# Optimization experiments

Hardware: AMD Instinct MI355X
Metric: run time of the kernel (lower is better)

## Reference

```python
import jax, jax.numpy as jnp
import numpy as np
from jax import lax

B, ENC, H, E, V = 16, 64, 96, 128, 32000

def _same_pad(k):
    # PyTorch padding='same' (stride=1): low = (k-1)//2, high = (k-1) - low
    t = k - 1
    return (t // 2, t - t // 2)

def _conv(x, w, pad):
    return lax.conv_general_dilated(x, w, (1, 1), pad,
                                    dimension_numbers=('NCHW', 'OIHW', 'NCHW'))

def setup_inputs() -> dict:
    key = jax.random.key(0)
    ks = jax.random.split(key, 16)
    s = 0.05
    return {
        'encoder_outputs': jax.random.normal(ks[0], (B, ENC, H), jnp.float32),
        'input_ids': jax.random.randint(ks[1], (B,), 0, V),
        'hidden': jax.random.normal(ks[2], (1, B, H), jnp.float32),
        'coverage': jnp.zeros((B, ENC), jnp.float32),
        'emb': jax.random.normal(ks[3], (V, E), jnp.float32) * s,
        'W_dec': jax.random.normal(ks[4], (H, H), jnp.float32) * s,
        'b_dec': jnp.zeros((H,), jnp.float32),
        'attn_w': jax.random.normal(ks[5], (ENC, ENC, H, H), jnp.float32) * 0.003,
        'attn_b': jnp.zeros((ENC,), jnp.float32),
        'cvg_w': jax.random.normal(ks[6], (ENC, ENC, 1, H), jnp.float32) * s,
        'cvg_b': jnp.zeros((ENC,), jnp.float32),
        'v': jax.random.normal(ks[7], (B, H), jnp.float32) * s,
        'W_new': jax.random.normal(ks[8], (H, H + E), jnp.float32) * s,
        'b_new': jnp.zeros((H,), jnp.float32),
        'w_ih': jax.random.normal(ks[9], (3 * H, H), jnp.float32) * s,
        'w_hh': jax.random.normal(ks[10], (3 * H, H), jnp.float32) * s,
        'b_ih': jnp.zeros((3 * H,), jnp.float32),
        'b_hh': jnp.zeros((3 * H,), jnp.float32),
        'W_pre': jax.random.normal(ks[11], (H, 2 * H), jnp.float32) * s,
        'b_pre': jnp.zeros((H,), jnp.float32),
        'W_out': jax.random.normal(ks[12], (V, H), jnp.float32) * s,
        'b_out': jnp.zeros((V,), jnp.float32),
    }

def _attn(hidden, enc_out, coverage, W_dec, b_dec, attn_w, attn_b, cvg_w, cvg_b, v):
    # AttnCalc.forward
    ph, pw = _same_pad(H), _same_pad(H)
    enc_feat = _conv(enc_out.reshape(B, ENC, 1, H), attn_w, (ph, pw))
    enc_feat = enc_feat + attn_b[None, :, None, None]          # (B,ENC,1,H)
    dec_feat = (hidden[0] @ W_dec.T + b_dec).reshape(B, 1, 1, H)
    cvg_feat = _conv(coverage.reshape(B, ENC, 1, 1), cvg_w, ((0, 0), _same_pad(H)))
    cvg_feat = cvg_feat + cvg_b[None, :, None, None]           # (B,ENC,1,1)
    feats = jnp.tanh((enc_feat + dec_feat + cvg_feat).reshape(B, ENC, H))
    attn_weights = jax.nn.softmax(jnp.einsum('beh,bh->be', feats, v), axis=1)
    new_cov = coverage + attn_weights                          # in-place += in torch
    ctx = jnp.einsum('be,beh->bh', attn_weights, enc_out)      # (B,H)
    return ctx, attn_weights, new_cov

def reference(encoder_outputs, input_ids, hidden, coverage, emb, W_dec, b_dec,
              attn_w, attn_b, cvg_w, cvg_b, v, W_new, b_new,
              w_ih, w_hh, b_ih, b_hh, W_pre, b_pre, W_out, b_out):
    embedded = emb[input_ids]                                  # (B,E); dropout = identity (eval)
    ctx1, _, cov1 = _attn(hidden, encoder_outputs, coverage,
                          W_dec, b_dec, attn_w, attn_b, cvg_w, cvg_b, v)
    x = jnp.concatenate([embedded, ctx1], axis=1) @ W_new.T + b_new   # (B,H)
    # single GRU step (PyTorch gate order: r, z, n)
    h = hidden[0]
    gi = x @ w_ih.T + b_ih
    gh = h @ w_hh.T + b_hh
    r = jax.nn.sigmoid(gi[:, :H] + gh[:, :H])
    z = jax.nn.sigmoid(gi[:, H:2 * H] + gh[:, H:2 * H])
    n = jnp.tanh(gi[:, 2 * H:] + r * gh[:, 2 * H:])
    h_new = (1.0 - z) * n + z * h                              # (B,H)
    hidden_new = h_new[None]                                   # (1,B,H)
    ctx2, aw2, cov2 = _attn(hidden_new, encoder_outputs, cov1,
                            W_dec, b_dec, attn_w, attn_b, cvg_w, cvg_b, v)
    o = jnp.tanh(jnp.concatenate([h_new, ctx2], axis=1) @ W_pre.T + b_pre)
    logp = jax.nn.log_softmax(o @ W_out.T + b_out, axis=1)     # (B,V)
    return (logp, hidden_new, ctx2, aw2, cov2)
```

## Files before the change

kernel.cpp:

```cpp
#include <hip/hip_runtime.h>

#define BB 16
#define ENC 64
#define HH 96
#define EE 128
#define VV 32000

__device__ __forceinline__ float tanh_fast(float x) {
    float e = __expf(2.f * x);
    return 1.f - 2.f / (e + 1.f);
}
__device__ __forceinline__ float sigmoid_fast(float x) {
    return 1.f / (1.f + __expf(-x));
}

__global__ __launch_bounds__(128) void k_encfeat(
    const float* __restrict__ enc,
    const float* __restrict__ attn_w,
    const float* __restrict__ cvg_w,
    float* __restrict__ part,
    float* __restrict__ cvgw47)
{
    int blk = blockIdx.x;
    int b   = blk >> 6;
    int ot  = (blk >> 3) & 7;
    int ic  = blk & 7;
    int o0  = ot * 8;
    int i0  = ic * 8;
    int t   = threadIdx.x;

    __shared__ __align__(16) float encS[8 * 192];
    __shared__ __align__(16) float Wb[8 * 8 * 100];

    for (int f = t; f < 8 * 192; f += 128) encS[f] = 0.f;
    __syncthreads();
    for (int f = t; f < 8 * 96; f += 128) {
        int i = f / 96, j = f - i * 96;
        encS[i * 192 + 47 + j] = enc[(size_t)((b * ENC + i0 + i) * 96) + j];
    }
    for (int f4 = t; f4 < 1536; f4 += 128) {
        int o = f4 / 192;
        int r = f4 - o * 192;
        int i = r / 24, kq = r - i * 24;
        float4 q = *(const float4*)(attn_w +
            (size_t)((o0 + o) * ENC + (i0 + i)) * (96 * 96) + 47 * 96 + 4 * kq);
        *(float4*)&Wb[(i * 8 + o) * 100 + 4 * kq] = q;
    }
    if (b == 0 && ot == 0) {
        #pragma unroll
        for (int j = 0; j < 4; ++j) {
            int e = ic * 512 + j * 128 + t;
            cvgw47[e] = cvg_w[(size_t)e * 96 + 47];
        }
    }
    __syncthreads();

    if (t < 96) {
        int og = t & 7;
        int x0 = (t >> 3) * 8;
        float4 a0 = make_float4(0.f, 0.f, 0.f, 0.f);
        float4 a1 = make_float4(0.f, 0.f, 0.f, 0.f);
        for (int i = 0; i < 8; ++i) {
            const float* er = &encS[i * 192 + x0];
            const float* wr = &Wb[(i * 8 + og) * 100];
            float4 eA = *(const float4*)(er);
            float4 eB = *(const float4*)(er + 4);
            #pragma unroll 4
            for (int c = 0; c < 24; ++c) {
                float4 eC = *(const float4*)(er + 4 * c + 8);
                float4 q  = *(const float4*)(wr + 4 * c);
                a0.x += q.x * eA.x + q.y * eA.y + q.z * eA.z + q.w * eA.w;
                a0.y += q.x * eA.y + q.y * eA.z + q.z * eA.w + q.w * eB.x;
                a0.z += q.x * eA.z + q.y * eA.w + q.z * eB.x + q.w * eB.y;
                a0.w += q.x * eA.w + q.y * eB.x + q.z * eB.y + q.w * eB.z;
                a1.x += q.x * eB.x + q.y * eB.y + q.z * eB.z + q.w * eB.w;
                a1.y += q.x * eB.y + q.y * eB.z + q.z * eB.w + q.w * eC.x;
                a1.z += q.x * eB.z + q.y * eB.w + q.z * eC.x + q.w * eC.y;
                a1.w += q.x * eB.w + q.y * eC.x + q.z * eC.y + q.w * eC.z;
                eA = eB; eB = eC;
            }
        }
        float* outr = part + ((size_t)(ic * 16 + b) * 64 + o0 + og) * 96 + x0;
        *(float4*)(outr)     = a0;
        *(float4*)(outr + 4) = a1;
    }
}

__device__ __forceinline__ void matvec4(int g, int q, int nout, int nk,
    const float* __restrict__ W, int ldw, const float* __restrict__ bias,
    const float* __restrict__ xv, float* __restrict__ y)
{
    for (int j = g; j < nout; j += 64) {
        const float* wr = W + (size_t)j * ldw;
        float s = 0.f;
        for (int m = q; m < nk / 4; m += 4) {
            float4 wq = *(const float4*)(wr + 4 * m);
            s += wq.x * xv[4 * m] + wq.y * xv[4 * m + 1]
               + wq.z * xv[4 * m + 2] + wq.w * xv[4 * m + 3];
        }
        s += __shfl_xor(s, 1);
        s += __shfl_xor(s, 2);
        if (q == 0) y[j] = s + bias[j];
    }
}

__global__ __launch_bounds__(256) void k_fused(
    const float* __restrict__ enc, const int* __restrict__ ids,
    const float* __restrict__ hidden, const float* __restrict__ coverage,
    const float* __restrict__ emb,
    const float* __restrict__ W_dec, const float* __restrict__ b_dec,
    const float* __restrict__ attn_b,
    const float* __restrict__ cvgw47, const float* __restrict__ cvg_b,
    const float* __restrict__ vvec,
    const float* __restrict__ W_new, const float* __restrict__ b_new,
    const float* __restrict__ w_ih, const float* __restrict__ w_hh,
    const float* __restrict__ b_ih, const float* __restrict__ b_hh,
    const float* __restrict__ W_pre, const float* __restrict__ b_pre,
    const float* __restrict__ part, float* __restrict__ oG,
    float* __restrict__ out_hidden, float* __restrict__ out_ctx2,
    float* __restrict__ out_aw2, float* __restrict__ out_cov2)
{
    int b = blockIdx.x, t = threadIdx.x;
    int g = t >> 2, q = t & 3;

    __shared__ __align__(16) float efS[ENC * HH];
    __shared__ __align__(16) float encS[ENC * HH];
    __shared__ float hS[HH], vS[HH], decS[HH], ctxS[HH], xS[HH], h2S[HH], ctx2S[HH];
    __shared__ float covS[ENC], cvgS[ENC], sS[ENC], awS[ENC];
    __shared__ float embS[EE];
    __shared__ __align__(16) float xcatS[EE + HH];
    __shared__ float giS[3 * HH], ghS[3 * HH];

    {
        const float4* enc4 = (const float4*)(enc + (size_t)b * ENC * HH);
        float4* efS4  = (float4*)efS;
        float4* encS4 = (float4*)encS;
        for (int f = t; f < (ENC * HH) / 4; f += 256) {
            float4 s = make_float4(0.f, 0.f, 0.f, 0.f);
            #pragma unroll
            for (int ic = 0; ic < 8; ++ic) {
                const float4 p = *(const float4*)(part +
                    (size_t)(ic * 16 + b) * (ENC * HH) + 4 * f);
                s.x += p.x; s.y += p.y; s.z += p.z; s.w += p.w;
            }
            efS4[f]  = s;
            encS4[f] = enc4[f];
        }
    }
    if (t < HH) { hS[t] = hidden[b * HH + t]; vS[t] = vvec[b * HH + t]; }
    if (t >= 96 && t < 160) covS[t - 96] = coverage[b * ENC + (t - 96)];
    if (t >= 128 && t < 256) embS[t - 128] = emb[(size_t)ids[b] * EE + (t - 128)];
    __syncthreads();

    matvec4(g, q, HH, HH, W_dec, HH, b_dec, hS, decS);
    matvec4(g, q, ENC, ENC, cvgw47, ENC, cvg_b, covS, cvgS);
    __syncthreads();
    {
        int e = g;
        float base = attn_b[e] + cvgS[e];
        const float* efr = &efS[e * HH];
        float s = 0.f;
        for (int m = q; m < 24; m += 4) {
            #pragma unroll
            for (int u = 0; u < 4; ++u) {
                int xx = 4 * m + u;
                s += tanh_fast(efr[xx] + decS[xx] + base) * vS[xx];
            }
        }
        s += __shfl_xor(s, 1); s += __shfl_xor(s, 2);
        if (q == 0) sS[e] = s;
    }
    __syncthreads();
    if (t < ENC) {
        float m = -1e30f;
        for (int j = 0; j < ENC; ++j) m = fmaxf(m, sS[j]);
        float sum = 0.f;
        for (int j = 0; j < ENC; ++j) sum += __expf(sS[j] - m);
        float aw = __expf(sS[t] - m) / sum;
        awS[t] = aw;
        covS[t] += aw;
    }
    __syncthreads();
    if (t < HH) {
        float c = 0.f;
        for (int o = 0; o < ENC; ++o) c += awS[o] * encS[o * HH + t];
        ctxS[t] = c;
        xcatS[EE + t] = c;
    }
    if (t >= 128 && t < 256) xcatS[t - 128] = embS[t - 128];
    __syncthreads();

    matvec4(g, q, HH, EE + HH, W_new, EE + HH, b_new, xcatS, xS);
    __syncthreads();

    matvec4(g, q, 3 * HH, HH, w_ih, HH, b_ih, xS, giS);
    matvec4(g, q, 3 * HH, HH, w_hh, HH, b_hh, hS, ghS);
    __syncthreads();
    if (t < HH) {
        float r = sigmoid_fast(giS[t] + ghS[t]);
        float z = sigmoid_fast(giS[HH + t] + ghS[HH + t]);
        float n = tanh_fast(giS[2 * HH + t] + r * ghS[2 * HH + t]);
        float hn = (1.f - z) * n + z * hS[t];
        h2S[t] = hn;
        out_hidden[b * HH + t] = hn;
    }
    __syncthreads();

    matvec4(g, q, HH, HH, W_dec, HH, b_dec, h2S, decS);
    matvec4(g, q, ENC, ENC, cvgw47, ENC, cvg_b, covS, cvgS);
    __syncthreads();
    {
        int e = g;
        float base = attn_b[e] + cvgS[e];
        const float* efr = &efS[e * HH];
        float s = 0.f;
        for (int m = q; m < 24; m += 4) {
            #pragma unroll
            for (int u = 0; u < 4; ++u) {
                int xx = 4 * m + u;
                s += tanh_fast(efr[xx] + decS[xx] + base) * vS[xx];
            }
        }
        s += __shfl_xor(s, 1); s += __shfl_xor(s, 2);
        if (q == 0) sS[e] = s;
    }
    __syncthreads();
    if (t < ENC) {
        float m = -1e30f;
        for (int j = 0; j < ENC; ++j) m = fmaxf(m, sS[j]);
        float sum = 0.f;
        for (int j = 0; j < ENC; ++j) sum += __expf(sS[j] - m);
        float aw = __expf(sS[t] - m) / sum;
        awS[t] = aw;
        covS[t] += aw;
        out_aw2[b * ENC + t]  = aw;
        out_cov2[b * ENC + t] = covS[t];
    }
    __syncthreads();
    if (t < HH) {
        float c = 0.f;
        for (int o = 0; o < ENC; ++o) c += awS[o] * encS[o * HH + t];
        ctx2S[t] = c;
        out_ctx2[b * HH + t] = c;
        xcatS[t] = h2S[t];
        xcatS[HH + t] = c;
    }
    __syncthreads();

    for (int j = g; j < HH; j += 64) {
        const float* wr = W_pre + (size_t)j * (2 * HH);
        float s = 0.f;
        for (int m = q; m < (2 * HH) / 4; m += 4) {
            float4 wq = *(const float4*)(wr + 4 * m);
            s += wq.x * xcatS[4 * m] + wq.y * xcatS[4 * m + 1]
               + wq.z * xcatS[4 * m + 2] + wq.w * xcatS[4 * m + 3];
        }
        s += __shfl_xor(s, 1); s += __shfl_xor(s, 2);
        if (q == 0) oG[b * HH + j] = tanh_fast(s + b_pre[j]);
    }
}

__global__ __launch_bounds__(128) void k_logits(
    const float* __restrict__ oG, const float* __restrict__ W_out,
    const float* __restrict__ b_out, float* __restrict__ logits)
{
    __shared__ __align__(16) float oS[BB * HH];
    for (int i = threadIdx.x; i < BB * HH; i += 128) oS[i] = oG[i];
    __syncthreads();

    int v = blockIdx.x * 128 + threadIdx.x;
    const float4* row = (const float4*)(W_out + (size_t)v * HH);
    float acc[BB];
    #pragma unroll
    for (int b = 0; b < BB; ++b) acc[b] = 0.f;

    #pragma unroll 6
    for (int c = 0; c < HH / 4; ++c) {
        float4 qv = row[c];
        #pragma unroll
        for (int b = 0; b < BB; ++b) {
            const float4 o0 = *(const float4*)&oS[b * HH + c * 4];
            acc[b] += qv.x * o0.x + qv.y * o0.y + qv.z * o0.z + qv.w * o0.w;
        }
    }
    float bo = b_out[v];
    #pragma unroll
    for (int b = 0; b < BB; ++b) logits[b * VV + v] = acc[b] + bo;
}

__global__ __launch_bounds__(1024) void k_logsoftmax(float* __restrict__ out)
{
    int b = blockIdx.x, t = threadIdx.x;
    float* row = out + (size_t)b * VV;
    __shared__ float red[1024];

    float m0 = -1e30f, m1 = -1e30f, m2 = -1e30f, m3 = -1e30f;
    int v = t;
    for (; v + 3072 < VV; v += 4096) {
        m0 = fmaxf(m0, row[v]);
        m1 = fmaxf(m1, row[v + 1024]);
        m2 = fmaxf(m2, row[v + 2048]);
        m3 = fmaxf(m3, row[v + 3072]);
    }
    for (; v < VV; v += 1024) m0 = fmaxf(m0, row[v]);
    red[t] = fmaxf(fmaxf(m0, m1), fmaxf(m2, m3));
    __syncthreads();
    for (int s = 512; s > 0; s >>= 1) {
        if (t < s) red[t] = fmaxf(red[t], red[t + s]);
        __syncthreads();
    }
    float m = red[0]; __syncthreads();

    float s0 = 0.f, s1 = 0.f, s2 = 0.f, s3 = 0.f;
    v = t;
    for (; v + 3072 < VV; v += 4096) {
        s0 += __expf(row[v] - m);
        s1 += __expf(row[v + 1024] - m);
        s2 += __expf(row[v + 2048] - m);
        s3 += __expf(row[v + 3072] - m);
    }
    for (; v < VV; v += 1024) s0 += __expf(row[v] - m);
    red[t] = (s0 + s1) + (s2 + s3);
    __syncthreads();
    for (int s = 512; s > 0; s >>= 1) {
        if (t < s) red[t] += red[t + s];
        __syncthreads();
    }
    float logZ = m + logf(red[0]);

    for (v = t; v < VV; v += 1024) row[v] = row[v] - logZ;
}

extern "C" void kernel_launch(void* const* d_in, const int* in_sizes, int n_in,
                              void* d_out, int out_size, void* d_ws, size_t ws_size,
                              hipStream_t stream) {
    const float* enc    = (const float*)d_in[0];
    const int*   ids    = (const int*)d_in[1];
    const float* hidden = (const float*)d_in[2];
    const float* cover  = (const float*)d_in[3];
    const float* emb    = (const float*)d_in[4];
    const float* W_dec  = (const float*)d_in[5];
    const float* b_dec  = (const float*)d_in[6];
    const float* attn_w = (const float*)d_in[7];
    const float* attn_b = (const float*)d_in[8];
    const float* cvg_w  = (const float*)d_in[9];
    const float* cvg_b  = (const float*)d_in[10];
    const float* vvec   = (const float*)d_in[11];
    const float* W_new  = (const float*)d_in[12];
    const float* b_new  = (const float*)d_in[13];
    const float* w_ih   = (const float*)d_in[14];
    const float* w_hh   = (const float*)d_in[15];
    const float* b_ih   = (const float*)d_in[16];
    const float* b_hh   = (const float*)d_in[17];
    const float* W_pre  = (const float*)d_in[18];
    const float* b_pre  = (const float*)d_in[19];
    const float* W_out  = (const float*)d_in[20];
    const float* b_out  = (const float*)d_in[21];

    float* wsf    = (float*)d_ws;
    float* oG     = wsf;
    float* cvgw47 = wsf + 1536;
    float* part   = wsf + 5632;

    float* out        = (float*)d_out;
    float* out_logp   = out;
    float* out_hidden = out + 512000;
    float* out_ctx2   = out + 513536;
    float* out_aw2    = out + 515072;
    float* out_cov2   = out + 516096;

    k_encfeat<<<1024, 128, 0, stream>>>(enc, attn_w, cvg_w, part, cvgw47);
    k_fused<<<16, 256, 0, stream>>>(enc, ids, hidden, cover, emb, W_dec, b_dec,
                                    attn_b, cvgw47, cvg_b, vvec, W_new, b_new,
                                    w_ih, w_hh, b_ih, b_hh, W_pre, b_pre,
                                    part, oG,
                                    out_hidden, out_ctx2, out_aw2, out_cov2);
    k_logits<<<250, 128, 0, stream>>>(oG, W_out, b_out, out_logp);
    k_logsoftmax<<<16, 1024, 0, stream>>>(out_logp);
}
```

Before: 346.3 us.

## Retile encoder conv kernel and keep log-softmax row in registers

The encoder feature kernel is retiled to 16 output channels by 4 input channels per block. All 128 threads now work, each computing 12 outputs, and the window loads are rotated. The reduction kernel sums 16 partials instead of 8, so it reads twice the partial buffer traffic. Log-softmax now loads each row once as float4 into registers and reuses them for max, sum and the final write, which removes two extra global passes over the logits.

```diff
diff --git a/kernel.cpp b/kernel.cpp
--- a/kernel.cpp
+++ b/kernel.cpp
@@ -13,6 +13,21 @@
 __device__ __forceinline__ float sigmoid_fast(float x) {
     return 1.f / (1.f + __expf(-x));
 }
+
+#define STEP(q, wa, wb_, wc_, wd_) do { \
+    accA.x += q.x*wa.x  + q.y*wa.y  + q.z*wa.z  + q.w*wa.w;  \
+    accA.y += q.x*wa.y  + q.y*wa.z  + q.z*wa.w  + q.w*wb_.x; \
+    accA.z += q.x*wa.z  + q.y*wa.w  + q.z*wb_.x + q.w*wb_.y; \
+    accA.w += q.x*wa.w  + q.y*wb_.x + q.z*wb_.y + q.w*wb_.z; \
+    accB.x += q.x*wb_.x + q.y*wb_.y + q.z*wb_.z + q.w*wb_.w; \
+    accB.y += q.x*wb_.y + q.y*wb_.z + q.z*wb_.w + q.w*wc_.x; \
+    accB.z += q.x*wb_.z + q.y*wb_.w + q.z*wc_.x + q.w*wc_.y; \
+    accB.w += q.x*wb_.w + q.y*wc_.x + q.z*wc_.y + q.w*wc_.z; \
+    accC.x += q.x*wc_.x + q.y*wc_.y + q.z*wc_.z + q.w*wc_.w; \
+    accC.y += q.x*wc_.y + q.y*wc_.z + q.z*wc_.w + q.w*wd_.x; \
+    accC.z += q.x*wc_.z + q.y*wc_.w + q.z*wd_.x + q.w*wd_.y; \
+    accC.w += q.x*wc_.w + q.y*wd_.x + q.z*wd_.y + q.w*wd_.z; \
+} while (0)
 
 __global__ __launch_bounds__(128) void k_encfeat(
     const float* __restrict__ enc,
@@ -23,30 +38,31 @@
 {
     int blk = blockIdx.x;
     int b   = blk >> 6;
-    int ot  = (blk >> 3) & 7;
-    int ic  = blk & 7;
-    int o0  = ot * 8;
-    int i0  = ic * 8;
+    int ot  = (blk >> 4) & 3;
+    int ic  = blk & 15;
+    int o0  = ot * 16;
+    int i0  = ic * 4;
     int t   = threadIdx.x;
 
-    __shared__ __align__(16) float encS[8 * 192];
-    __shared__ __align__(16) float Wb[8 * 8 * 100];
-
-    for (int f = t; f < 8 * 192; f += 128) encS[f] = 0.f;
-    __syncthreads();
-    for (int f = t; f < 8 * 96; f += 128) {
+    __shared__ __align__(16) float encS[4 * 208];
+    __shared__ __align__(16) float Wb[4 * 16 * 100];
+
+    for (int f = t; f < 208; f += 128)
+        ((float4*)encS)[f] = make_float4(0.f, 0.f, 0.f, 0.f);
+    __syncthreads();
+    for (int f = t; f < 4 * 96; f += 128) {
         int i = f / 96, j = f - i * 96;
-        encS[i * 192 + 47 + j] = enc[(size_t)((b * ENC + i0 + i) * 96) + j];
-    }
-    for (int f4 = t; f4 < 1536; f4 += 128) {
-        int o = f4 / 192;
-        int r = f4 - o * 192;
+        encS[i * 208 + 47 + j] = enc[(size_t)((b * ENC + i0 + i) * 96) + j];
+    }
+    for (int F = t; F < 1536; F += 128) {
+        int o = F / 96;
+        int r = F - o * 96;
         int i = r / 24, kq = r - i * 24;
         float4 q = *(const float4*)(attn_w +
             (size_t)((o0 + o) * ENC + (i0 + i)) * (96 * 96) + 47 * 96 + 4 * kq);
-        *(float4*)&Wb[(i * 8 + o) * 100 + 4 * kq] = q;
-    }
-    if (b == 0 && ot == 0) {
+        *(float4*)&Wb[(i * 16 + o) * 100 + 4 * kq] = q;
+    }
+    if (b == 0 && ot == 0 && ic < 8) {
         #pragma unroll
         for (int j = 0; j < 4; ++j) {
             int e = ic * 512 + j * 128 + t;
@@ -55,35 +71,44 @@
     }
     __syncthreads();
 
-    if (t < 96) {
-        int og = t & 7;
-        int x0 = (t >> 3) * 8;
-        float4 a0 = make_float4(0.f, 0.f, 0.f, 0.f);
-        float4 a1 = make_float4(0.f, 0.f, 0.f, 0.f);
-        for (int i = 0; i < 8; ++i) {
-            const float* er = &encS[i * 192 + x0];
-            const float* wr = &Wb[(i * 8 + og) * 100];
-            float4 eA = *(const float4*)(er);
-            float4 eB = *(const float4*)(er + 4);
-            #pragma unroll 4
-            for (int c = 0; c < 24; ++c) {
-                float4 eC = *(const float4*)(er + 4 * c + 8);
-                float4 q  = *(const float4*)(wr + 4 * c);
-                a0.x += q.x * eA.x + q.y * eA.y + q.z * eA.z + q.w * eA.w;
-                a0.y += q.x * eA.y + q.y * eA.z + q.z * eA.w + q.w * eB.x;
-                a0.z += q.x * eA.z + q.y * eA.w + q.z * eB.x + q.w * eB.y;
-                a0.w += q.x * eA.w + q.y * eB.x + q.z * eB.y + q.w * eB.z;
-                a1.x += q.x * eB.x + q.y * eB.y + q.z * eB.z + q.w * eB.w;
-                a1.y += q.x * eB.y + q.y * eB.z + q.z * eB.w + q.w * eC.x;
-                a1.z += q.x * eB.z + q.y * eB.w + q.z * eC.x + q.w * eC.y;
-                a1.w += q.x * eB.w + q.y * eC.x + q.z * eC.y + q.w * eC.z;
-                eA = eB; eB = eC;
-            }
-        }
-        float* outr = part + ((size_t)(ic * 16 + b) * 64 + o0 + og) * 96 + x0;
-        *(float4*)(outr)     = a0;
-        *(float4*)(outr + 4) = a1;
-    }
+    int w    = t >> 6;
+    int ln   = t & 63;
+    int og   = ln & 7;
+    int xs   = ln >> 3;
+    int x0   = xs * 12;
+    int orow = w * 8 + og;
+
+    float4 accA = make_float4(0.f, 0.f, 0.f, 0.f);
+    float4 accB = make_float4(0.f, 0.f, 0.f, 0.f);
+    float4 accC = make_float4(0.f, 0.f, 0.f, 0.f);
+
+    for (int i = 0; i < 4; ++i) {
+        const float* er = &encS[i * 208 + x0];
+        const float* wr = &Wb[(i * 16 + orow) * 100];
+        float4 e0 = *(const float4*)(er);
+        float4 e1 = *(const float4*)(er + 4);
+        float4 e2 = *(const float4*)(er + 8);
+        float4 e3 = *(const float4*)(er + 12);
+        #pragma unroll
+        for (int cb = 0; cb < 6; ++cb) {
+            float4 q0 = *(const float4*)(wr + 16 * cb);
+            float4 q1 = *(const float4*)(wr + 16 * cb + 4);
+            float4 q2 = *(const float4*)(wr + 16 * cb + 8);
+            float4 q3 = *(const float4*)(wr + 16 * cb + 12);
+            STEP(q0, e0, e1, e2, e3);
+            e0 = *(const float4*)(er + 16 * cb + 16);
+            STEP(q1, e1, e2, e3, e0);
+            e1 = *(const float4*)(er + 16 * cb + 20);
+            STEP(q2, e2, e3, e0, e1);
+            e2 = *(const float4*)(er + 16 * cb + 24);
+            STEP(q3, e3, e0, e1, e2);
+            e3 = *(const float4*)(er + 16 * cb + 28);
+        }
+    }
+    float* outr = part + ((size_t)(ic * 16 + b) * 64 + o0 + orow) * 96 + x0;
+    *(float4*)(outr)     = accA;
+    *(float4*)(outr + 4) = accB;
+    *(float4*)(outr + 8) = accC;
 }
 
 __device__ __forceinline__ void matvec4(int g, int q, int nout, int nk,
@@ -138,7 +163,7 @@
         for (int f = t; f < (ENC * HH) / 4; f += 256) {
             float4 s = make_float4(0.f, 0.f, 0.f, 0.f);
             #pragma unroll
-            for (int ic = 0; ic < 8; ++ic) {
+            for (int ic = 0; ic < 16; ++ic) {
                 const float4 p = *(const float4*)(part +
                     (size_t)(ic * 16 + b) * (ENC * HH) + 4 * f);
                 s.x += p.x; s.y += p.y; s.z += p.z; s.w += p.w;
@@ -288,22 +313,29 @@
     for (int b = 0; b < BB; ++b) logits[b * VV + v] = acc[b] + bo;
 }
 
+#define MAX4(r) fmaxf(fmaxf((r).x, (r).y), fmaxf((r).z, (r).w))
 __global__ __launch_bounds__(1024) void k_logsoftmax(float* __restrict__ out)
 {
     int b = blockIdx.x, t = threadIdx.x;
     float* row = out + (size_t)b * VV;
+    const float4* row4 = (const float4*)row;
+    float4* row4w = (float4*)row;
     __shared__ float red[1024];
 
-    float m0 = -1e30f, m1 = -1e30f, m2 = -1e30f, m3 = -1e30f;
-    int v = t;
-    for (; v + 3072 < VV; v += 4096) {
-        m0 = fmaxf(m0, row[v]);
-        m1 = fmaxf(m1, row[v + 1024]);
-        m2 = fmaxf(m2, row[v + 2048]);
-        m3 = fmaxf(m3, row[v + 3072]);
-    }
-    for (; v < VV; v += 1024) m0 = fmaxf(m0, row[v]);
-    red[t] = fmaxf(fmaxf(m0, m1), fmaxf(m2, m3));
+    float4 c0, c1, c2, c3, c4, c5, c6, c7;
+    bool has7 = (t < 8000 - 7 * 1024);
+    c0 = row4[t];
+    c1 = row4[t + 1024];
+    c2 = row4[t + 2048];
+    c3 = row4[t + 3072];
+    c4 = row4[t + 4096];
+    c5 = row4[t + 5120];
+    c6 = row4[t + 6144];
+    float m0 = fmaxf(fmaxf(MAX4(c0), MAX4(c1)),
+                     fmaxf(fmaxf(MAX4(c2), MAX4(c3)),
+                           fmaxf(MAX4(c4), fmaxf(MAX4(c5), MAX4(c6)))));
+    if (has7) { c7 = row4[t + 7168]; m0 = fmaxf(m0, MAX4(c7)); }
+    red[t] = m0;
     __syncthreads();
     for (int s = 512; s > 0; s >>= 1) {
         if (t < s) red[t] = fmaxf(red[t], red[t + s]);
@@ -311,16 +343,13 @@
     }
     float m = red[0]; __syncthreads();
 
-    float s0 = 0.f, s1 = 0.f, s2 = 0.f, s3 = 0.f;
-    v = t;
-    for (; v + 3072 < VV; v += 4096) {
-        s0 += __expf(row[v] - m);
-        s1 += __expf(row[v + 1024] - m);
-        s2 += __expf(row[v + 2048] - m);
-        s3 += __expf(row[v + 3072] - m);
-    }
-    for (; v < VV; v += 1024) s0 += __expf(row[v] - m);
-    red[t] = (s0 + s1) + (s2 + s3);
+    float s0 = 0.f;
+    #define ESUM(r) (__expf((r).x - m) + __expf((r).y - m) + \
+                     __expf((r).z - m) + __expf((r).w - m))
+    s0 = ESUM(c0) + ESUM(c1) + ESUM(c2) + ESUM(c3)
+       + ESUM(c4) + ESUM(c5) + ESUM(c6);
+    if (has7) s0 += ESUM(c7);
+    red[t] = s0;
     __syncthreads();
     for (int s = 512; s > 0; s >>= 1) {
         if (t < s) red[t] += red[t + s];
@@ -328,7 +357,16 @@
     }
     float logZ = m + logf(red[0]);
 
-    for (v = t; v < VV; v += 1024) row[v] = row[v] - logZ;
+    #define SUB4(r) { (r).x -= logZ; (r).y -= logZ; (r).z -= logZ; (r).w -= logZ; }
+    SUB4(c0); SUB4(c1); SUB4(c2); SUB4(c3); SUB4(c4); SUB4(c5); SUB4(c6);
+    row4w[t]        = c0;
+    row4w[t + 1024] = c1;
+    row4w[t + 2048] = c2;
+    row4w[t + 3072] = c3;
+    row4w[t + 4096] = c4;
+    row4w[t + 5120] = c5;
+    row4w[t + 6144] = c6;
+    if (has7) { SUB4(c7); row4w[t + 7168] = c7; }
 }
 
 extern "C" void kernel_launch(void* const* d_in, const int* in_sizes, int n_in,
```

Result: no change. 345.2 us (-0.3%).
